# Kernel optimization log

Measured on AMD Instinct MI355X. Metric: run time of the kernel, lower is better.

Reference implementation:

```python
import jax, jax.numpy as jnp
import numpy as np

B, C, H, W = 4, 128, 128, 128
HEADS, DHEAD = 8, C // 8
N = H * W
NEG_SLOPE = 0.2
LN_EPS = 1e-5


def _build_grid_edges(h, w):
    # 3x3 neighborhood including self (matches the torch double loop),
    # then append N extra self loops (add_self_loops in the module).
    rows, cols = [], []
    for r in range(h):
        for c in range(w):
            idx = r * w + c
            for dr in (-1, 0, 1):
                for dc in (-1, 0, 1):
                    nr, nc = r + dr, c + dc
                    if 0 <= nr < h and 0 <= nc < w:
                        rows.append(idx)
                        cols.append(nr * w + nc)
    rows += list(range(h * w))
    cols += list(range(h * w))
    return np.asarray(rows, np.int32), np.asarray(cols, np.int32)

_SRC_NP, _DST_NP = _build_grid_edges(H, W)  # PyG: messages flow src -> dst
SRC = jnp.asarray(_SRC_NP)
DST = jnp.asarray(_DST_NP)


def setup_inputs() -> dict:
    key = jax.random.key(0)
    ks = jax.random.split(key, 7)
    s_lin = 1.0 / np.sqrt(C)
    return {
        "x": jax.random.normal(ks[0], (B, C, H, W), jnp.float32),
        "W_lin": jax.random.normal(ks[1], (C, HEADS * DHEAD), jnp.float32) * s_lin,
        "att_src": jax.random.normal(ks[2], (HEADS, DHEAD), jnp.float32) * s_lin,
        "att_dst": jax.random.normal(ks[3], (HEADS, DHEAD), jnp.float32) * s_lin,
        "bias": jnp.zeros((C,), jnp.float32),
        "gamma": jnp.ones((C,), jnp.float32),
        "beta": jnp.zeros((C,), jnp.float32),
    }


def _gat_forward(x, W_lin, att_src, att_dst, bias, gamma, beta):
    b = x.shape[0]
    x_nodes = x.reshape(b, C, N).transpose(0, 2, 1)            # [B,N,C]
    xp = (x_nodes @ W_lin).reshape(b, N, HEADS, DHEAD)          # [B,N,H,D]
    a_src = jnp.einsum('bnhd,hd->bnh', xp, att_src)             # [B,N,H]
    a_dst = jnp.einsum('bnhd,hd->bnh', xp, att_dst)
    score = jax.nn.leaky_relu(a_src[:, SRC] + a_dst[:, DST], NEG_SLOPE)  # [B,E,H]

    def seg_softmax(s):  # [E,H] softmax over edges grouped by DST
        m = jax.ops.segment_max(s, DST, num_segments=N)
        e = jnp.exp(s - m[DST])
        den = jax.ops.segment_sum(e, DST, num_segments=N)
        return e / den[DST]

    alpha = jax.vmap(seg_softmax)(score)                        # [B,E,H]
    msg = xp[:, SRC] * alpha[..., None]                         # [B,E,H,D]
    agg = jax.vmap(lambda m: jax.ops.segment_sum(m, DST, num_segments=N))(msg)
    out = agg.reshape(b, N, C) + bias                           # GATConv bias
    out = jax.nn.elu(out)
    # LayerNorm over channel dim
    mu = out.mean(-1, keepdims=True)
    var = out.var(-1, keepdims=True)
    out = (out - mu) * jax.lax.rsqrt(var + LN_EPS) * gamma + beta
    return out.transpose(0, 2, 1).reshape(b, C, H, W)


def reference(x, W_lin, att_src, att_dst, bias, gamma, beta):
    return _gat_forward(x, W_lin, att_src, att_dst, bias, gamma, beta)
```

## Files before the change

### kernel.cpp

```cpp
#include <hip/hip_runtime.h>
#include <stdint.h>

#define BATCH  4
#define CCH    128
#define GRID_H 128
#define GRID_W 128
#define NNODE  (GRID_H*GRID_W)
#define NHEAD  8
#define DH     16
#define WPAD   68
#define WROWS  144

typedef __attribute__((ext_vector_type(8))) short short8;
typedef __attribute__((ext_vector_type(4))) float f32x4;
typedef __attribute__((ext_vector_type(4))) unsigned u32x4;

__device__ inline unsigned short f2bf(float f){
    unsigned u = __float_as_uint(f);
    return (unsigned short)((u + 0x7FFFu + ((u >> 16) & 1u)) >> 16);
}
__device__ inline unsigned packbf(float a, float b){
    return (unsigned)f2bf(a) | ((unsigned)f2bf(b) << 16);
}
__device__ inline float bflo(unsigned u){ return __uint_as_float(u << 16); }
__device__ inline float bfhi(unsigned u){ return __uint_as_float(u & 0xFFFF0000u); }

__global__ void kW(const float* __restrict__ Wl, const float* __restrict__ attS,
                   const float* __restrict__ attD, unsigned* __restrict__ Wb)
{
    __shared__ float Wa[8][16];
    const int t = threadIdx.x;
    const int cbase = blockIdx.x * 8;
    if (t < 128){
        int cl = t >> 4, j = t & 15;
        const float* av = (j < 8 ? attS + j*DH : attD + (j-8)*DH);
        const float* wr = Wl + (size_t)(cbase + cl)*CCH + (j & 7)*DH;
        float s = 0.f;
        #pragma unroll
        for (int d = 0; d < DH; ++d) s += wr[d]*av[d];
        Wa[cl][j] = s;
    }
    __syncthreads();
    for (int it = 0; it < 3; ++it){
        int flat = it*256 + t;
        if (flat < 576){
            int k2l = flat / 144, co = flat % 144;
            int k2 = blockIdx.x*4 + k2l;
            float w0, w1;
            if (co < CCH){
                w0 = Wl[(size_t)(2*k2)*CCH + co];
                w1 = Wl[(size_t)(2*k2+1)*CCH + co];
            } else {
                w0 = Wa[2*k2l][co-CCH];
                w1 = Wa[2*k2l+1][co-CCH];
            }
            Wb[co*WPAD + k2] = packbf(w0, w1);
        }
    }
}

__global__ __launch_bounds__(256, 3) void kA(
    const float* __restrict__ x, const unsigned* __restrict__ Wbg,
    unsigned short* __restrict__ xpb, float* __restrict__ scb)
{
    __shared__ __align__(16) unsigned WbL[WROWS*WPAD];

    const int t  = threadIdx.x;
    const int b  = blockIdx.y;
    const int n0 = blockIdx.x * 128;

    #pragma unroll
    for (int it = 0; it < 10; ++it){
        int f4 = it*256 + t;
        if (f4 < (WROWS*WPAD)/4)
            *(u32x4*)(&WbL[f4*4]) = *(const u32x4*)(Wbg + (size_t)f4*4);
    }
    __syncthreads();

    const int w = t >> 6, lane = t & 63;
    const int col = lane & 15, q = lane >> 4;
    const float* xb = x + (size_t)b*CCH*NNODE;
    const int nA = n0 + (2*w+0)*16 + col;
    const int nB = n0 + (2*w+1)*16 + col;

    f32x4 acc[2][9];
    #pragma unroll
    for (int mi = 0; mi < 2; ++mi)
        #pragma unroll
        for (int ct = 0; ct < 9; ++ct) acc[mi][ct] = (f32x4)(0.f);

    float xrA[8], xrB[8], x2A[8], x2B[8];
    #pragma unroll
    for (int j = 0; j < 8; ++j){
        const size_t co = (size_t)(q*8 + j)*NNODE;
        xrA[j] = xb[co + nA];
        xrB[j] = xb[co + nB];
    }

    union U { u32x4 u; short8 s; };
    #pragma unroll
    for (int kc = 0; kc < 4; ++kc){
        if (kc < 3){
            #pragma unroll
            for (int j = 0; j < 8; ++j){
                const size_t co = (size_t)((kc+1)*32 + q*8 + j)*NNODE;
                x2A[j] = xb[co + nA];
                x2B[j] = xb[co + nB];
            }
        }
        U fa0, fa1;
        #pragma unroll
        for (int i = 0; i < 4; ++i){
            fa0.u[i] = packbf(xrA[2*i], xrA[2*i+1]);
            fa1.u[i] = packbf(xrB[2*i], xrB[2*i+1]);
        }
        const int kof = kc*16 + q*4;
        #pragma unroll
        for (int ct = 0; ct < 9; ++ct){
            U fb; fb.u = *(const u32x4*)(&WbL[(ct*16+col)*WPAD + kof]);
            acc[0][ct] = __builtin_amdgcn_mfma_f32_16x16x32_bf16(fa0.s, fb.s, acc[0][ct], 0, 0, 0);
            acc[1][ct] = __builtin_amdgcn_mfma_f32_16x16x32_bf16(fa1.s, fb.s, acc[1][ct], 0, 0, 0);
        }
        #pragma unroll
        for (int j = 0; j < 8; ++j){ xrA[j] = x2A[j]; xrB[j] = x2B[j]; }
    }

    unsigned short* xr = xpb + (size_t)b*NNODE*CCH;
    float*          sr = scb + (size_t)b*NNODE*16;
    const int sidx = (col < 8) ? 2*col : 2*(col-8)+1;
    #pragma unroll
    for (int mi = 0; mi < 2; ++mi){
        #pragma unroll
        for (int r = 0; r < 4; ++r){
            const int n = n0 + (2*w+mi)*16 + q*4 + r;
            #pragma unroll
            for (int ct = 0; ct < 8; ++ct)
                xr[(size_t)n*CCH + ct*16 + col] = f2bf(acc[mi][ct][r]);
            sr[(size_t)n*16 + sidx] = acc[mi][8][r];
        }
    }
}

__device__ inline void kb_issue(int n, const float2* __restrict__ scB,
                                const uint2* __restrict__ xvb, int h, int l2,
                                int* vm, float2 sc[9], uint2 xv[9])
{
    const int rr = n >> 7, cc = n & 127;
    const bool vU = rr > 0, vD = rr < GRID_H-1, vL = cc > 0, vR = cc < GRID_W-1;
    int m = 0;
    #pragma unroll
    for (int e = 0; e < 9; ++e){
        const int dr = e/3 - 1, dc = e%3 - 1;
        const bool vr_ = (dr < 0) ? vU : (dr > 0 ? vD : true);
        const bool vc_ = (dc < 0) ? vL : (dc > 0 ? vR : true);
        const bool v = vr_ && vc_;
        const int src = v ? (n + dr*GRID_W + dc) : n;
        m |= ((int)v) << e;
        sc[e] = scB[src*8 + h];
        xv[e] = xvb[(size_t)src*32 + l2];
    }
    *vm = m;
}

__global__ __launch_bounds__(256, 3) void kB(
    const unsigned short* __restrict__ xpb, const float* __restrict__ scb,
    const float* __restrict__ bias, const float* __restrict__ gamma,
    const float* __restrict__ beta, float* __restrict__ out)
{
    __shared__ float outT[CCH][65];
    const int t = threadIdx.x, w = t >> 6, lane = t & 63;
    const int h2 = lane >> 5, l2 = lane & 31;
    const int b  = blockIdx.y;
    const int n0 = blockIdx.x * 64;
    const uint2*  xvb = (const uint2*)(xpb + (size_t)b*NNODE*CCH);
    const float2* scB = (const float2*)(scb + (size_t)b*NNODE*16);
    const int h = l2 >> 2;
    const f32x4 bi = *(const f32x4*)(bias  + 4*l2);
    const f32x4 ga = *(const f32x4*)(gamma + 4*l2);
    const f32x4 be = *(const f32x4*)(beta  + 4*l2);

    float2 scP[2][9]; uint2 xvP[2][9]; int vmP[2];

    #define NODE(i) (n0 + w*16 + 2*(i) + h2)
    kb_issue(NODE(0), scB, xvb, h, l2, &vmP[0], scP[0], xvP[0]);

    #pragma unroll
    for (int ii = 0; ii < 4; ++ii){
        #pragma unroll
        for (int ph = 0; ph < 2; ++ph){
            const int i = 2*ii + ph;
            const int cur = i & 1;
            if (i + 1 < 8)
                kb_issue(NODE(i+1), scB, xvb, h, l2, &vmP[cur^1], scP[cur^1], xvP[cur^1]);

            const int vm = vmP[cur];
            const float2* sc = scP[cur];
            const uint2*  xv = xvP[cur];
            const int nl = w*16 + 2*i + h2;

            const float ad = sc[4].y;
            float s[9], mx = -1e30f;
            #pragma unroll
            for (int e = 0; e < 9; ++e){
                float sv = sc[e].x + ad;
                sv = fmaxf(sv, 0.2f*sv);
                s[e] = ((vm >> e) & 1) ? sv : -1e30f;
                mx = fmaxf(mx, s[e]);
            }
            float wt[9], den = 0.f;
            #pragma unroll
            for (int e = 0; e < 9; ++e){
                float ex = __expf(s[e] - mx);
                ex = ((vm >> e) & 1) ? ex : 0.f;
                wt[e] = ex; den += ex;
            }
            den += wt[4];
            const float inv = __builtin_amdgcn_rcpf(den);

            float a0 = 0.f, a1 = 0.f, a2 = 0.f, a3 = 0.f;
            #pragma unroll
            for (int e = 0; e < 9; ++e){
                float f = wt[e] * inv;
                if (e == 4) f += f;
                a0 += f * bflo(xv[e].x);
                a1 += f * bfhi(xv[e].x);
                a2 += f * bflo(xv[e].y);
                a3 += f * bfhi(xv[e].y);
            }

            float o0 = a0 + bi[0], o1 = a1 + bi[1], o2 = a2 + bi[2], o3 = a3 + bi[3];
            o0 = o0 > 0.f ? o0 : __expf(o0) - 1.f;
            o1 = o1 > 0.f ? o1 : __expf(o1) - 1.f;
            o2 = o2 > 0.f ? o2 : __expf(o2) - 1.f;
            o3 = o3 > 0.f ? o3 : __expf(o3) - 1.f;

            float sm = (o0 + o1) + (o2 + o3);
            float sq = o0*o0 + o1*o1 + o2*o2 + o3*o3;
            #pragma unroll
            for (int off = 1; off <= 16; off <<= 1){
                sm += __shfl_xor(sm, off, 64);
                sq += __shfl_xor(sq, off, 64);
            }
            const float mu  = sm * (1.f/128.f);
            float var = sq * (1.f/128.f) - mu*mu;
            var = var < 0.f ? 0.f : var;
            const float rstd = __builtin_amdgcn_rsqf(var + 1e-5f);
            outT[4*l2+0][nl] = (o0 - mu)*rstd*ga[0] + be[0];
            outT[4*l2+1][nl] = (o1 - mu)*rstd*ga[1] + be[1];
            outT[4*l2+2][nl] = (o2 - mu)*rstd*ga[2] + be[2];
            outT[4*l2+3][nl] = (o3 - mu)*rstd*ga[3] + be[3];
        }
    }
    #undef NODE
    __syncthreads();

    float* ob = out + (size_t)b*CCH*NNODE + n0;
    #pragma unroll
    for (int it = 0; it < 32; ++it){
        int c = it*4 + w;
        ob[(size_t)c*NNODE + lane] = outT[c][lane];
    }
}

extern "C" void kernel_launch(void* const* d_in, const int* in_sizes, int n_in,
                              void* d_out, int out_size, void* d_ws, size_t ws_size,
                              hipStream_t stream)
{
    const float* x    = (const float*)d_in[0];
    const float* Wl   = (const float*)d_in[1];
    const float* attS = (const float*)d_in[2];
    const float* attD = (const float*)d_in[3];
    const float* bias = (const float*)d_in[4];
    const float* gamma= (const float*)d_in[5];
    const float* beta = (const float*)d_in[6];
    float* out = (float*)d_out;

    unsigned short* xpb = (unsigned short*)d_ws;
    float*          scb = (float*)(xpb + (size_t)BATCH*NNODE*CCH);
    unsigned*       Wb  = (unsigned*)(scb + (size_t)BATCH*NNODE*16);

    kW<<<dim3(16), 256, 0, stream>>>(Wl, attS, attD, Wb);
    kA<<<dim3(NNODE/128, BATCH), 256, 0, stream>>>(x, Wb, xpb, scb);
    kB<<<dim3(NNODE/64, BATCH), 256, 0, stream>>>(xpb, scb, bias, gamma, beta, out);
}
```

Baseline: 118.0 us.

## Stage neighbor halo tile in LDS and transpose MFMA operands for packed stores

The aggregation kernel now loads a 3x66-node halo of projected features into shared memory once per block and reads the 9 neighbors from LDS, instead of issuing 9 global gathers per node. The projection kernel swaps the A/B MFMA operands so each lane holds 4 consecutive channels of one node, which allows packed 8-byte bf16 stores and contiguous score stores. The softmax drops the explicit max subtraction. Risks are overflow in exp without the max shift, lower occupancy from the larger LDS footprint (about 50KB), and an extra barrier before the transpose.

```diff
diff --git a/kernel.cpp b/kernel.cpp
--- a/kernel.cpp
+++ b/kernel.cpp
@@ -80,8 +80,8 @@
     const int w = t >> 6, lane = t & 63;
     const int col = lane & 15, q = lane >> 4;
     const float* xb = x + (size_t)b*CCH*NNODE;
-    const int nA = n0 + (2*w+0)*16 + col;
-    const int nB = n0 + (2*w+1)*16 + col;
+    const int nA = n0 + 2*w*16 + col;
+    const int nB = nA + 16;
 
     f32x4 acc[2][9];
     #pragma unroll
@@ -108,18 +108,18 @@
                 x2B[j] = xb[co + nB];
             }
         }
-        U fa0, fa1;
+        U fb0, fb1;
         #pragma unroll
         for (int i = 0; i < 4; ++i){
-            fa0.u[i] = packbf(xrA[2*i], xrA[2*i+1]);
-            fa1.u[i] = packbf(xrB[2*i], xrB[2*i+1]);
+            fb0.u[i] = packbf(xrA[2*i], xrA[2*i+1]);
+            fb1.u[i] = packbf(xrB[2*i], xrB[2*i+1]);
         }
         const int kof = kc*16 + q*4;
         #pragma unroll
         for (int ct = 0; ct < 9; ++ct){
-            U fb; fb.u = *(const u32x4*)(&WbL[(ct*16+col)*WPAD + kof]);
-            acc[0][ct] = __builtin_amdgcn_mfma_f32_16x16x32_bf16(fa0.s, fb.s, acc[0][ct], 0, 0, 0);
-            acc[1][ct] = __builtin_amdgcn_mfma_f32_16x16x32_bf16(fa1.s, fb.s, acc[1][ct], 0, 0, 0);
+            U fa; fa.u = *(const u32x4*)(&WbL[(ct*16+col)*WPAD + kof]);
+            acc[0][ct] = __builtin_amdgcn_mfma_f32_16x16x32_bf16(fa.s, fb0.s, acc[0][ct], 0, 0, 0);
+            acc[1][ct] = __builtin_amdgcn_mfma_f32_16x16x32_bf16(fa.s, fb1.s, acc[1][ct], 0, 0, 0);
         }
         #pragma unroll
         for (int j = 0; j < 8; ++j){ xrA[j] = x2A[j]; xrB[j] = x2B[j]; }
@@ -127,39 +127,20 @@
 
     unsigned short* xr = xpb + (size_t)b*NNODE*CCH;
     float*          sr = scb + (size_t)b*NNODE*16;
-    const int sidx = (col < 8) ? 2*col : 2*(col-8)+1;
     #pragma unroll
     for (int mi = 0; mi < 2; ++mi){
-        #pragma unroll
-        for (int r = 0; r < 4; ++r){
-            const int n = n0 + (2*w+mi)*16 + q*4 + r;
-            #pragma unroll
-            for (int ct = 0; ct < 8; ++ct)
-                xr[(size_t)n*CCH + ct*16 + col] = f2bf(acc[mi][ct][r]);
-            sr[(size_t)n*16 + sidx] = acc[mi][8][r];
-        }
-    }
-}
-
-__device__ inline void kb_issue(int n, const float2* __restrict__ scB,
-                                const uint2* __restrict__ xvb, int h, int l2,
-                                int* vm, float2 sc[9], uint2 xv[9])
-{
-    const int rr = n >> 7, cc = n & 127;
-    const bool vU = rr > 0, vD = rr < GRID_H-1, vL = cc > 0, vR = cc < GRID_W-1;
-    int m = 0;
-    #pragma unroll
-    for (int e = 0; e < 9; ++e){
-        const int dr = e/3 - 1, dc = e%3 - 1;
-        const bool vr_ = (dr < 0) ? vU : (dr > 0 ? vD : true);
-        const bool vc_ = (dc < 0) ? vL : (dc > 0 ? vR : true);
-        const bool v = vr_ && vc_;
-        const int src = v ? (n + dr*GRID_W + dc) : n;
-        m |= ((int)v) << e;
-        sc[e] = scB[src*8 + h];
-        xv[e] = xvb[(size_t)src*32 + l2];
-    }
-    *vm = m;
+        const int n = mi ? nB : nA;
+        #pragma unroll
+        for (int ct = 0; ct < 8; ++ct){
+            uint2 p;
+            p.x = packbf(acc[mi][ct][0], acc[mi][ct][1]);
+            p.y = packbf(acc[mi][ct][2], acc[mi][ct][3]);
+            *(uint2*)(xr + (size_t)n*CCH + ct*16 + q*4) = p;
+        }
+        #pragma unroll
+        for (int r = 0; r < 4; ++r)
+            sr[(size_t)n*16 + q*4 + r] = acc[mi][8][r];
+    }
 }
 
 __global__ __launch_bounds__(256, 3) void kB(
@@ -167,98 +148,125 @@
     const float* __restrict__ bias, const float* __restrict__ gamma,
     const float* __restrict__ beta, float* __restrict__ out)
 {
-    __shared__ float outT[CCH][65];
+    __shared__ __align__(16) unsigned char SM[198*256];
     const int t = threadIdx.x, w = t >> 6, lane = t & 63;
     const int h2 = lane >> 5, l2 = lane & 31;
     const int b  = blockIdx.y;
     const int n0 = blockIdx.x * 64;
-    const uint2*  xvb = (const uint2*)(xpb + (size_t)b*NNODE*CCH);
-    const float2* scB = (const float2*)(scb + (size_t)b*NNODE*16);
+    const int r0 = n0 >> 7, c0 = n0 & 127;
+
+    {
+        const u32x4* xg = (const u32x4*)(xpb + (size_t)b*NNODE*CCH);
+        u32x4* xl = (u32x4*)SM;
+        for (int u = t; u < 198*16; u += 256){
+            int row = u >> 4, sub = u & 15;
+            int rr = row / 66, cc = row - rr*66;
+            int sr_ = r0 - 1 + rr; sr_ = sr_ < 0 ? 0 : (sr_ > 127 ? 127 : sr_);
+            int sc_ = c0 - 1 + cc; sc_ = sc_ < 0 ? 0 : (sc_ > 127 ? 127 : sc_);
+            xl[u] = xg[(size_t)(sr_*GRID_W + sc_)*16 + sub];
+        }
+    }
+    __syncthreads();
+
     const int h = l2 >> 2;
     const f32x4 bi = *(const f32x4*)(bias  + 4*l2);
     const f32x4 ga = *(const f32x4*)(gamma + 4*l2);
     const f32x4 be = *(const f32x4*)(beta  + 4*l2);
-
-    float2 scP[2][9]; uint2 xvP[2][9]; int vmP[2];
-
-    #define NODE(i) (n0 + w*16 + 2*(i) + h2)
-    kb_issue(NODE(0), scB, xvb, h, l2, &vmP[0], scP[0], xvP[0]);
-
-    #pragma unroll
-    for (int ii = 0; ii < 4; ++ii){
-        #pragma unroll
-        for (int ph = 0; ph < 2; ++ph){
-            const int i = 2*ii + ph;
-            const int cur = i & 1;
-            if (i + 1 < 8)
-                kb_issue(NODE(i+1), scB, xvb, h, l2, &vmP[cur^1], scP[cur^1], xvP[cur^1]);
-
-            const int vm = vmP[cur];
-            const float2* sc = scP[cur];
-            const uint2*  xv = xvP[cur];
-            const int nl = w*16 + 2*i + h2;
-
-            const float ad = sc[4].y;
-            float s[9], mx = -1e30f;
-            #pragma unroll
-            for (int e = 0; e < 9; ++e){
-                float sv = sc[e].x + ad;
-                sv = fmaxf(sv, 0.2f*sv);
-                s[e] = ((vm >> e) & 1) ? sv : -1e30f;
-                mx = fmaxf(mx, s[e]);
-            }
-            float wt[9], den = 0.f;
-            #pragma unroll
-            for (int e = 0; e < 9; ++e){
-                float ex = __expf(s[e] - mx);
-                ex = ((vm >> e) & 1) ? ex : 0.f;
-                wt[e] = ex; den += ex;
-            }
-            den += wt[4];
-            const float inv = __builtin_amdgcn_rcpf(den);
-
-            float a0 = 0.f, a1 = 0.f, a2 = 0.f, a3 = 0.f;
-            #pragma unroll
-            for (int e = 0; e < 9; ++e){
-                float f = wt[e] * inv;
-                if (e == 4) f += f;
-                a0 += f * bflo(xv[e].x);
-                a1 += f * bfhi(xv[e].x);
-                a2 += f * bflo(xv[e].y);
-                a3 += f * bfhi(xv[e].y);
-            }
-
-            float o0 = a0 + bi[0], o1 = a1 + bi[1], o2 = a2 + bi[2], o3 = a3 + bi[3];
-            o0 = o0 > 0.f ? o0 : __expf(o0) - 1.f;
-            o1 = o1 > 0.f ? o1 : __expf(o1) - 1.f;
-            o2 = o2 > 0.f ? o2 : __expf(o2) - 1.f;
-            o3 = o3 > 0.f ? o3 : __expf(o3) - 1.f;
-
-            float sm = (o0 + o1) + (o2 + o3);
-            float sq = o0*o0 + o1*o1 + o2*o2 + o3*o3;
-            #pragma unroll
-            for (int off = 1; off <= 16; off <<= 1){
-                sm += __shfl_xor(sm, off, 64);
-                sq += __shfl_xor(sq, off, 64);
-            }
-            const float mu  = sm * (1.f/128.f);
-            float var = sq * (1.f/128.f) - mu*mu;
-            var = var < 0.f ? 0.f : var;
-            const float rstd = __builtin_amdgcn_rsqf(var + 1e-5f);
-            outT[4*l2+0][nl] = (o0 - mu)*rstd*ga[0] + be[0];
-            outT[4*l2+1][nl] = (o1 - mu)*rstd*ga[1] + be[1];
-            outT[4*l2+2][nl] = (o2 - mu)*rstd*ga[2] + be[2];
-            outT[4*l2+3][nl] = (o3 - mu)*rstd*ga[3] + be[3];
-        }
-    }
-    #undef NODE
+    const float* scB = scb + (size_t)b*NNODE*16;
+
+    float oacc[8][4];
+    float aP[2][9], adP[2]; int vmP[2];
+
+    #define ISSUE(i, buf) { \
+        const int nl_ = w*16 + 2*(i) + h2, n_ = n0 + nl_; \
+        const int rr_ = n_ >> 7, cc_ = n_ & 127; \
+        int m_ = 0; \
+        _Pragma("unroll") \
+        for (int e = 0; e < 9; ++e){ \
+            const int dr = e/3 - 1, dc = e%3 - 1; \
+            const bool v = ((unsigned)(rr_+dr) < GRID_H) && ((unsigned)(cc_+dc) < GRID_W); \
+            const int src = v ? (n_ + dr*GRID_W + dc) : n_; \
+            m_ |= ((int)v) << e; \
+            aP[buf][e] = scB[(size_t)src*16 + h]; \
+        } \
+        adP[buf] = scB[(size_t)n_*16 + 8 + h]; \
+        vmP[buf] = m_; }
+
+    ISSUE(0, 0)
+    #pragma unroll
+    for (int i = 0; i < 8; ++i){
+        const int cur = i & 1;
+        if (i < 7) ISSUE(i+1, cur^1)
+        const int nl = w*16 + 2*i + h2;
+        const int vm = vmP[cur];
+        const float ad = adP[cur];
+
+        float wt[9], den = 0.f;
+        #pragma unroll
+        for (int e = 0; e < 9; ++e){
+            float sv = aP[cur][e] + ad;
+            sv = fmaxf(sv, 0.2f*sv);
+            sv = ((vm >> e) & 1) ? sv : -1e30f;
+            float ex = __expf(sv);
+            wt[e] = ex; den += ex;
+        }
+        den += wt[4];
+        const float inv = __builtin_amdgcn_rcpf(den);
+
+        float a0 = 0.f, a1 = 0.f, a2 = 0.f, a3 = 0.f;
+        #pragma unroll
+        for (int e = 0; e < 9; ++e){
+            const int dr = e/3 - 1, dc = e%3 - 1;
+            float f = wt[e] * inv;
+            if (e == 4) f += f;
+            const int row = (dr+1)*66 + nl + 1 + dc;
+            const uint2 xv = *(const uint2*)(SM + row*256 + 8*l2);
+            a0 += f * bflo(xv.x);
+            a1 += f * bfhi(xv.x);
+            a2 += f * bflo(xv.y);
+            a3 += f * bfhi(xv.y);
+        }
+
+        float o0 = a0 + bi[0], o1 = a1 + bi[1], o2 = a2 + bi[2], o3 = a3 + bi[3];
+        o0 = o0 > 0.f ? o0 : __expf(o0) - 1.f;
+        o1 = o1 > 0.f ? o1 : __expf(o1) - 1.f;
+        o2 = o2 > 0.f ? o2 : __expf(o2) - 1.f;
+        o3 = o3 > 0.f ? o3 : __expf(o3) - 1.f;
+
+        float sm = (o0 + o1) + (o2 + o3);
+        float sq = o0*o0 + o1*o1 + o2*o2 + o3*o3;
+        #pragma unroll
+        for (int off = 1; off <= 16; off <<= 1){
+            sm += __shfl_xor(sm, off, 64);
+            sq += __shfl_xor(sq, off, 64);
+        }
+        const float mu  = sm * (1.f/128.f);
+        float var = sq * (1.f/128.f) - mu*mu;
+        var = var < 0.f ? 0.f : var;
+        const float rstd = __builtin_amdgcn_rsqf(var + 1e-5f);
+        oacc[i][0] = (o0 - mu)*rstd*ga[0] + be[0];
+        oacc[i][1] = (o1 - mu)*rstd*ga[1] + be[1];
+        oacc[i][2] = (o2 - mu)*rstd*ga[2] + be[2];
+        oacc[i][3] = (o3 - mu)*rstd*ga[3] + be[3];
+    }
+    #undef ISSUE
+    __syncthreads();
+
+    float* oT = (float*)SM;
+    #pragma unroll
+    for (int i = 0; i < 8; ++i){
+        const int nl = w*16 + 2*i + h2;
+        #pragma unroll
+        for (int k = 0; k < 4; ++k)
+            oT[(4*l2 + k)*67 + nl] = oacc[i][k];
+    }
     __syncthreads();
 
     float* ob = out + (size_t)b*CCH*NNODE + n0;
     #pragma unroll
     for (int it = 0; it < 32; ++it){
-        int c = it*4 + w;
-        ob[(size_t)c*NNODE + lane] = outT[c][lane];
+        const int c = it*4 + w;
+        ob[(size_t)c*NNODE + lane] = oT[c*67 + lane];
     }
 }
 
```

After: 126.4 us. 1.07x slower.

## Swap MFMA operands for vectorized projection stores, drop softmax max, raise occupancy

Applied to the files above, without the earlier changes.

The projection kernel now feeds W as the A operand and node features as the B operand. Each lane therefore holds four consecutive channels of a single node, so the bf16 features go out as 8-byte stores and the scores as contiguous floats, instead of scattered 2-byte writes. The score layout becomes [src heads | dst heads] per node, and the aggregation kernel reads the destination term with a separate load. The edge softmax no longer subtracts the running max, which saves a reduction pass but can overflow if scores grow large. The aggregation kernel's launch bounds are raised from 3 to 4 blocks per CU, which trades register budget for occupancy.

```diff
diff --git a/kernel.cpp b/kernel.cpp
--- a/kernel.cpp
+++ b/kernel.cpp
@@ -80,8 +80,8 @@
     const int w = t >> 6, lane = t & 63;
     const int col = lane & 15, q = lane >> 4;
     const float* xb = x + (size_t)b*CCH*NNODE;
-    const int nA = n0 + (2*w+0)*16 + col;
-    const int nB = n0 + (2*w+1)*16 + col;
+    const int nA = n0 + 2*w*16 + col;
+    const int nB = nA + 16;
 
     f32x4 acc[2][9];
     #pragma unroll
@@ -108,18 +108,18 @@
                 x2B[j] = xb[co + nB];
             }
         }
-        U fa0, fa1;
+        U fb0, fb1;
         #pragma unroll
         for (int i = 0; i < 4; ++i){
-            fa0.u[i] = packbf(xrA[2*i], xrA[2*i+1]);
-            fa1.u[i] = packbf(xrB[2*i], xrB[2*i+1]);
+            fb0.u[i] = packbf(xrA[2*i], xrA[2*i+1]);
+            fb1.u[i] = packbf(xrB[2*i], xrB[2*i+1]);
         }
         const int kof = kc*16 + q*4;
         #pragma unroll
         for (int ct = 0; ct < 9; ++ct){
-            U fb; fb.u = *(const u32x4*)(&WbL[(ct*16+col)*WPAD + kof]);
-            acc[0][ct] = __builtin_amdgcn_mfma_f32_16x16x32_bf16(fa0.s, fb.s, acc[0][ct], 0, 0, 0);
-            acc[1][ct] = __builtin_amdgcn_mfma_f32_16x16x32_bf16(fa1.s, fb.s, acc[1][ct], 0, 0, 0);
+            U fa; fa.u = *(const u32x4*)(&WbL[(ct*16+col)*WPAD + kof]);
+            acc[0][ct] = __builtin_amdgcn_mfma_f32_16x16x32_bf16(fa.s, fb0.s, acc[0][ct], 0, 0, 0);
+            acc[1][ct] = __builtin_amdgcn_mfma_f32_16x16x32_bf16(fa.s, fb1.s, acc[1][ct], 0, 0, 0);
         }
         #pragma unroll
         for (int j = 0; j < 8; ++j){ xrA[j] = x2A[j]; xrB[j] = x2B[j]; }
@@ -127,23 +127,25 @@
 
     unsigned short* xr = xpb + (size_t)b*NNODE*CCH;
     float*          sr = scb + (size_t)b*NNODE*16;
-    const int sidx = (col < 8) ? 2*col : 2*(col-8)+1;
     #pragma unroll
     for (int mi = 0; mi < 2; ++mi){
-        #pragma unroll
-        for (int r = 0; r < 4; ++r){
-            const int n = n0 + (2*w+mi)*16 + q*4 + r;
-            #pragma unroll
-            for (int ct = 0; ct < 8; ++ct)
-                xr[(size_t)n*CCH + ct*16 + col] = f2bf(acc[mi][ct][r]);
-            sr[(size_t)n*16 + sidx] = acc[mi][8][r];
-        }
-    }
-}
-
-__device__ inline void kb_issue(int n, const float2* __restrict__ scB,
+        const int n = mi ? nB : nA;
+        #pragma unroll
+        for (int ct = 0; ct < 8; ++ct){
+            uint2 p;
+            p.x = packbf(acc[mi][ct][0], acc[mi][ct][1]);
+            p.y = packbf(acc[mi][ct][2], acc[mi][ct][3]);
+            *(uint2*)(xr + (size_t)n*CCH + ct*16 + q*4) = p;
+        }
+        #pragma unroll
+        for (int r = 0; r < 4; ++r)
+            sr[(size_t)n*16 + q*4 + r] = acc[mi][8][r];
+    }
+}
+
+__device__ inline void kb_issue(int n, const float* __restrict__ scB,
                                 const uint2* __restrict__ xvb, int h, int l2,
-                                int* vm, float2 sc[9], uint2 xv[9])
+                                int* vm, float* ad, float sc[9], uint2 xv[9])
 {
     const int rr = n >> 7, cc = n & 127;
     const bool vU = rr > 0, vD = rr < GRID_H-1, vL = cc > 0, vR = cc < GRID_W-1;
@@ -156,13 +158,14 @@
         const bool v = vr_ && vc_;
         const int src = v ? (n + dr*GRID_W + dc) : n;
         m |= ((int)v) << e;
-        sc[e] = scB[src*8 + h];
+        sc[e] = scB[(size_t)src*16 + h];
         xv[e] = xvb[(size_t)src*32 + l2];
     }
+    *ad = scB[(size_t)n*16 + 8 + h];
     *vm = m;
 }
 
-__global__ __launch_bounds__(256, 3) void kB(
+__global__ __launch_bounds__(256, 4) void kB(
     const unsigned short* __restrict__ xpb, const float* __restrict__ scb,
     const float* __restrict__ bias, const float* __restrict__ gamma,
     const float* __restrict__ beta, float* __restrict__ out)
@@ -172,84 +175,74 @@
     const int h2 = lane >> 5, l2 = lane & 31;
     const int b  = blockIdx.y;
     const int n0 = blockIdx.x * 64;
-    const uint2*  xvb = (const uint2*)(xpb + (size_t)b*NNODE*CCH);
-    const float2* scB = (const float2*)(scb + (size_t)b*NNODE*16);
+    const uint2* xvb = (const uint2*)(xpb + (size_t)b*NNODE*CCH);
+    const float* scB = scb + (size_t)b*NNODE*16;
     const int h = l2 >> 2;
     const f32x4 bi = *(const f32x4*)(bias  + 4*l2);
     const f32x4 ga = *(const f32x4*)(gamma + 4*l2);
     const f32x4 be = *(const f32x4*)(beta  + 4*l2);
 
-    float2 scP[2][9]; uint2 xvP[2][9]; int vmP[2];
+    float scP[2][9]; uint2 xvP[2][9]; float adP[2]; int vmP[2];
 
     #define NODE(i) (n0 + w*16 + 2*(i) + h2)
-    kb_issue(NODE(0), scB, xvb, h, l2, &vmP[0], scP[0], xvP[0]);
-
-    #pragma unroll
-    for (int ii = 0; ii < 4; ++ii){
-        #pragma unroll
-        for (int ph = 0; ph < 2; ++ph){
-            const int i = 2*ii + ph;
-            const int cur = i & 1;
-            if (i + 1 < 8)
-                kb_issue(NODE(i+1), scB, xvb, h, l2, &vmP[cur^1], scP[cur^1], xvP[cur^1]);
-
-            const int vm = vmP[cur];
-            const float2* sc = scP[cur];
-            const uint2*  xv = xvP[cur];
-            const int nl = w*16 + 2*i + h2;
-
-            const float ad = sc[4].y;
-            float s[9], mx = -1e30f;
-            #pragma unroll
-            for (int e = 0; e < 9; ++e){
-                float sv = sc[e].x + ad;
-                sv = fmaxf(sv, 0.2f*sv);
-                s[e] = ((vm >> e) & 1) ? sv : -1e30f;
-                mx = fmaxf(mx, s[e]);
-            }
-            float wt[9], den = 0.f;
-            #pragma unroll
-            for (int e = 0; e < 9; ++e){
-                float ex = __expf(s[e] - mx);
-                ex = ((vm >> e) & 1) ? ex : 0.f;
-                wt[e] = ex; den += ex;
-            }
-            den += wt[4];
-            const float inv = __builtin_amdgcn_rcpf(den);
-
-            float a0 = 0.f, a1 = 0.f, a2 = 0.f, a3 = 0.f;
-            #pragma unroll
-            for (int e = 0; e < 9; ++e){
-                float f = wt[e] * inv;
-                if (e == 4) f += f;
-                a0 += f * bflo(xv[e].x);
-                a1 += f * bfhi(xv[e].x);
-                a2 += f * bflo(xv[e].y);
-                a3 += f * bfhi(xv[e].y);
-            }
-
-            float o0 = a0 + bi[0], o1 = a1 + bi[1], o2 = a2 + bi[2], o3 = a3 + bi[3];
-            o0 = o0 > 0.f ? o0 : __expf(o0) - 1.f;
-            o1 = o1 > 0.f ? o1 : __expf(o1) - 1.f;
-            o2 = o2 > 0.f ? o2 : __expf(o2) - 1.f;
-            o3 = o3 > 0.f ? o3 : __expf(o3) - 1.f;
-
-            float sm = (o0 + o1) + (o2 + o3);
-            float sq = o0*o0 + o1*o1 + o2*o2 + o3*o3;
-            #pragma unroll
-            for (int off = 1; off <= 16; off <<= 1){
-                sm += __shfl_xor(sm, off, 64);
-                sq += __shfl_xor(sq, off, 64);
-            }
-            const float mu  = sm * (1.f/128.f);
-            float var = sq * (1.f/128.f) - mu*mu;
-            var = var < 0.f ? 0.f : var;
-            const float rstd = __builtin_amdgcn_rsqf(var + 1e-5f);
-            outT[4*l2+0][nl] = (o0 - mu)*rstd*ga[0] + be[0];
-            outT[4*l2+1][nl] = (o1 - mu)*rstd*ga[1] + be[1];
-            outT[4*l2+2][nl] = (o2 - mu)*rstd*ga[2] + be[2];
-            outT[4*l2+3][nl] = (o3 - mu)*rstd*ga[3] + be[3];
-        }
+    kb_issue(NODE(0), scB, xvb, h, l2, &vmP[0], &adP[0], scP[0], xvP[0]);
+
+    #pragma unroll
+    for (int i = 0; i < 8; ++i){
+        const int cur = i & 1;
+        if (i < 7)
+            kb_issue(NODE(i+1), scB, xvb, h, l2, &vmP[cur^1], &adP[cur^1], scP[cur^1], xvP[cur^1]);
+
+        const int vm = vmP[cur];
+        const float* sc = scP[cur];
+        const uint2* xv = xvP[cur];
+        const float ad = adP[cur];
+        const int nl = w*16 + 2*i + h2;
+
+        float wt[9], den = 0.f;
+        #pragma unroll
+        for (int e = 0; e < 9; ++e){
+            float sv = sc[e] + ad;
+            sv = fmaxf(sv, 0.2f*sv);
+            sv = ((vm >> e) & 1) ? sv : -1e30f;
+            float ex = __expf(sv);
+            wt[e] = ex; den += ex;
+        }
+        den += wt[4];
+        const float inv = __builtin_amdgcn_rcpf(den);
+
+        float a0 = 0.f, a1 = 0.f, a2 = 0.f, a3 = 0.f;
+        #pragma unroll
+        for (int e = 0; e < 9; ++e){
+            float f = wt[e] * inv;
+            if (e == 4) f += f;
+            a0 += f * bflo(xv[e].x);
+            a1 += f * bfhi(xv[e].x);
+            a2 += f * bflo(xv[e].y);
+            a3 += f * bfhi(xv[e].y);
+        }
+
+        float o0 = a0 + bi[0], o1 = a1 + bi[1], o2 = a2 + bi[2], o3 = a3 + bi[3];
+        o0 = o0 > 0.f ? o0 : __expf(o0) - 1.f;
+        o1 = o1 > 0.f ? o1 : __expf(o1) - 1.f;
+        o2 = o2 > 0.f ? o2 : __expf(o2) - 1.f;
+        o3 = o3 > 0.f ? o3 : __expf(o3) - 1.f;
+
+        float sm = (o0 + o1) + (o2 + o3);
+        float sq = o0*o0 + o1*o1 + o2*o2 + o3*o3;
+        #pragma unroll
+        for (int off = 1; off <= 16; off <<= 1){
+            sm += __shfl_xor(sm, off, 64);
+            sq += __shfl_xor(sq, off, 64);
+        }
+        const float mu  = sm * (1.f/128.f);
+        float var = sq * (1.f/128.f) - mu*mu;
+        var = var < 0.f ? 0.f : var;
+        const float rstd = __builtin_amdgcn_rsqf(var + 1e-5f);
+        outT[4*l2+0][nl] = (o0 - mu)*rstd*ga[0] + be[0];
+        outT[4*l2+1][nl] = (o1 - mu)*rstd*ga[1] + be[1];
+        outT[4*l2+2][nl] = (o2 - mu)*rstd*ga[2] + be[2];
+        outT[4*l2+3][nl] = (o3 - mu)*rstd*ga[3] + be[3];
     }
     #undef NODE
     __syncthreads();
@@ -257,7 +250,7 @@
     float* ob = out + (size_t)b*CCH*NNODE + n0;
     #pragma unroll
     for (int it = 0; it < 32; ++it){
-        int c = it*4 + w;
+        const int c = it*4 + w;
         ob[(size_t)c*NNODE + lane] = outT[c][lane];
     }
 }
```

New measurement: 125.5 us. +6.3%, slower.
